# Kernel optimization log

Measured on AMD Instinct MI355X. Metric: run time of the kernel, lower is better.

Reference implementation:

```python
import jax, jax.numpy as jnp
import numpy as np

D_MODEL = 2048
N_Q_HEADS = 32
N_KV_HEADS = 8
D_HEAD = 64
D_MLP = 8192
NORM_EPS = 1e-5
INIT_RANGE = 0.02
IGNORE = -100000.0
B, S = 2, 2048


def setup_inputs() -> dict:
    key = jax.random.key(0)
    ks = jax.random.split(key, 8)
    return {
        "resid_pre": jax.random.normal(ks[0], (B, S, D_MODEL), dtype=jnp.float32),
        "W_Q": jax.random.normal(ks[1], (N_Q_HEADS, D_MODEL, D_HEAD), dtype=jnp.float32) * INIT_RANGE,
        "W_K": jax.random.normal(ks[2], (N_KV_HEADS, D_MODEL, D_HEAD), dtype=jnp.float32) * INIT_RANGE,
        "W_V": jax.random.normal(ks[3], (N_KV_HEADS, D_MODEL, D_HEAD), dtype=jnp.float32) * INIT_RANGE,
        "W_O": jax.random.normal(ks[4], (N_KV_HEADS, D_HEAD, D_MODEL), dtype=jnp.float32) * INIT_RANGE,
        "g1": jnp.ones((D_MODEL,), jnp.float32),
        "b1": jnp.zeros((D_MODEL,), jnp.float32),
        "g2": jnp.ones((D_MODEL,), jnp.float32),
        "b2": jnp.zeros((D_MODEL,), jnp.float32),
        "W_in": jax.random.normal(ks[5], (D_MODEL, D_MLP), dtype=jnp.float32) * INIT_RANGE,
        "b_in": jnp.zeros((D_MLP,), jnp.float32),
        "W_out": jax.random.normal(ks[6], (D_MLP, D_MODEL), dtype=jnp.float32) * INIT_RANGE,
        "b_out": jnp.zeros((D_MODEL,), jnp.float32),
    }


def rmsnorm(x, g, b):
    # torch.var (unbiased=False) is mean-centered variance, but x itself is
    # divided (not centered) -- faithful to the source.
    mu = jnp.mean(x, axis=-1, keepdims=True)
    var = jnp.mean(jnp.square(x - mu), axis=-1, keepdims=True)
    std = jnp.sqrt(var + NORM_EPS)
    return (x / std) * g + b


def attention(x, W_Q, W_K, W_V, W_O):
    b, s, _ = x.shape
    q = jnp.einsum('bpd,hde->bphe', x, W_Q)            # [b, s, n_q, d_head]
    k = jnp.einsum('bpd,hde->bphe', x, W_K)            # [b, s, n_kv, d_head]
    v = jnp.einsum('bpd,hde->bphe', x, W_V)            # [b, s, n_kv, d_head]
    g_size = N_Q_HEADS // N_KV_HEADS
    # rearrange '(n_kv g) d' with n_kv outer, group inner
    q = q.reshape(b, s, N_KV_HEADS, g_size, D_HEAD)
    # source einsum sums over the group dim (g not in output) -- faithful
    scores = jnp.einsum('bqkgd,bskd->bkqs', q, k) / jnp.sqrt(jnp.float32(D_HEAD))
    mask = jnp.triu(jnp.ones((s, s), dtype=bool), k=1)
    scores = jnp.where(mask, jnp.float32(IGNORE), scores)
    pattern = jax.nn.softmax(scores, axis=-1)          # [b, n_kv, q, s]
    z = jnp.einsum('bskd,bkqs->bqkd', v, pattern)      # [b, q, n_kv, d_head]
    return jnp.einsum('bqkd,kde->bqe', z, W_O)


def ffn(x, W_in, b_in, W_out, b_out):
    pre = jnp.einsum('bpd,dm->bpm', x, W_in) + b_in
    post = jax.nn.relu(pre)
    return jnp.einsum('bpm,md->bpd', post, W_out) + b_out


def reference(resid_pre, W_Q, W_K, W_V, W_O, g1, b1, g2, b2, W_in, b_in, W_out, b_out):
    resid_mid = attention(rmsnorm(resid_pre, g1, b1), W_Q, W_K, W_V, W_O) + resid_pre
    resid_post = ffn(rmsnorm(resid_mid, g2, b2), W_in, b_in, W_out, b_out) + resid_mid
    return resid_post
```

## Files before the change

### kernel.cpp

```cpp
#include <hip/hip_runtime.h>
#include <hip/hip_bf16.h>


using bf16 = __hip_bfloat16;
typedef __bf16 bf16x8_t __attribute__((ext_vector_type(8)));
typedef float  f32x4_t  __attribute__((ext_vector_type(4)));

#define D_MODEL 2048
#define SEQ     2048
#define NB      2
#define NTOK    4096
#define NKV     8
#define DHEAD   64
#define DMLP    8192
#define NQKV    1536

__device__ inline void storev(float* p, float v) { *p = v; }
__device__ inline void storev(bf16* p, float v)  { *p = __float2bfloat16(v); }

__device__ inline __bf16 tobf(float x) {
    union { __hip_bfloat16 h; __bf16 b; } u;
    u.h = __float2bfloat16(x);
    return u.b;
}

__global__ __launch_bounds__(256) void transpose_f32_bf16_kernel(
    const float* __restrict__ in, bf16* __restrict__ out, int K, int N)
{
    __shared__ float tile[32][33];
    const int n0 = blockIdx.x * 32, k0 = blockIdx.y * 32;
    const int tx = threadIdx.x & 31, ty = threadIdx.x >> 5;
    #pragma unroll
    for (int i = 0; i < 32; i += 8)
        tile[ty + i][tx] = in[(size_t)(k0 + ty + i) * N + n0 + tx];
    __syncthreads();
    #pragma unroll
    for (int i = 0; i < 32; i += 8)
        out[(size_t)(n0 + ty + i) * K + k0 + tx] = __float2bfloat16(tile[tx][ty + i]);
}

__global__ __launch_bounds__(256) void head_transpose_kernel(
    const float* __restrict__ in, bf16* __restrict__ out, int ngroup)
{
    __shared__ float tile[32][65];
    const int kv = blockIdx.y;
    const int k0 = blockIdx.x * 32;
    const int t  = threadIdx.x;
    const int e  = t & 63, kk = t >> 6;
    #pragma unroll
    for (int i = 0; i < 32; i += 4) {
        float s = 0.f;
        for (int g = 0; g < ngroup; ++g)
            s += in[((size_t)(kv * ngroup + g) * 2048 + k0 + kk + i) * 64 + e];
        tile[kk + i][e] = s;
    }
    __syncthreads();
    const int k = t & 31, ee = t >> 5;
    #pragma unroll
    for (int i = 0; i < 64; i += 8)
        out[(size_t)(kv * 64 + ee + i) * 2048 + k0 + k] = __float2bfloat16(tile[k][ee + i]);
}

__global__ __launch_bounds__(256) void rmsnorm_kernel(
    const float* __restrict__ x, const float* __restrict__ g,
    const float* __restrict__ b, bf16* __restrict__ out)
{
    const int row = blockIdx.x;
    const int t = threadIdx.x;
    const float* xr = x + (size_t)row * D_MODEL;
    float4 a0 = *reinterpret_cast<const float4*>(xr + t * 8);
    float4 a1 = *reinterpret_cast<const float4*>(xr + t * 8 + 4);
    float v[8] = {a0.x, a0.y, a0.z, a0.w, a1.x, a1.y, a1.z, a1.w};
    float sum = 0.f, sumsq = 0.f;
    #pragma unroll
    for (int j = 0; j < 8; ++j) { sum += v[j]; sumsq += v[j] * v[j]; }
    #pragma unroll
    for (int o = 1; o < 64; o <<= 1) {
        sum   += __shfl_xor(sum, o);
        sumsq += __shfl_xor(sumsq, o);
    }
    __shared__ float rs[4], rq[4];
    if ((t & 63) == 0) { rs[t >> 6] = sum; rq[t >> 6] = sumsq; }
    __syncthreads();
    sum   = rs[0] + rs[1] + rs[2] + rs[3];
    sumsq = rq[0] + rq[1] + rq[2] + rq[3];
    const float mu  = sum * (1.f / D_MODEL);
    const float var = sumsq * (1.f / D_MODEL) - mu * mu;
    const float rstd = 1.f / sqrtf(var + 1e-5f);
    const int c = t * 8;
    float4 g0 = *reinterpret_cast<const float4*>(g + c);
    float4 g1 = *reinterpret_cast<const float4*>(g + c + 4);
    float4 b0 = *reinterpret_cast<const float4*>(b + c);
    float4 b1 = *reinterpret_cast<const float4*>(b + c + 4);
    float gg[8] = {g0.x, g0.y, g0.z, g0.w, g1.x, g1.y, g1.z, g1.w};
    float bb[8] = {b0.x, b0.y, b0.z, b0.w, b1.x, b1.y, b1.z, b1.w};
    bf16* op = out + (size_t)row * D_MODEL + c;
    #pragma unroll
    for (int j = 0; j < 8; ++j) op[j] = __float2bfloat16(v[j] * rstd * gg[j] + bb[j]);
}

template<int BM, int BN, typename TC, bool BIAS, bool RELU, bool RESID>
__global__ __launch_bounds__(512, 2) void gemm_pipe_kernel(
    const bf16* __restrict__ A, const bf16* __restrict__ Bt,
    TC* __restrict__ C, const float* __restrict__ bias,
    const float* __restrict__ resid, int M, int N, int K, int nbx)
{
    constexpr int BK   = 64;
    constexpr int MREP = BM / 32;
    constexpr int NREP = BN / 64;
    constexpr int AI   = (BM * BK) / 4096;
    constexpr int BI   = (BN * BK) / 4096;
    constexpr int LD   = AI + BI;

    __shared__ __align__(16) bf16 As[2][BM * BK];
    __shared__ __align__(16) bf16 Bs[2][BN * BK];

    const int nwg = gridDim.x;
    const int swz = (blockIdx.x & 7) * (nwg >> 3) + (blockIdx.x >> 3);
    const int nby = nwg / nbx;
    const int by  = swz % nby;
    const int bx  = swz / nby;
    const int row0 = by * BM, col0 = bx * BN;

    const int t  = threadIdx.x;
    const int w  = t >> 6, ln = t & 63;
    const int wm = w >> 2, wn = w & 3;
    const int lr = ln & 15, hi = ln >> 4;

    const int srow = w * 8 + (ln >> 3);
    const int skx  = ((ln & 7) ^ (ln >> 3)) * 8;

    f32x4_t acc[MREP][NREP];
    #pragma unroll
    for (int m = 0; m < MREP; ++m)
        #pragma unroll
        for (int n = 0; n < NREP; ++n) acc[m][n] = (f32x4_t){0.f, 0.f, 0.f, 0.f};

    const int NT = K / BK;

    {
        const bf16* ga = A  + (size_t)(row0 + srow) * K + skx;
        const bf16* gb = Bt + (size_t)(col0 + srow) * K + skx;
        #pragma unroll
        for (int i = 0; i < AI; ++i)
            __builtin_amdgcn_global_load_lds(
                (const __attribute__((address_space(1))) void*)(ga + (size_t)i * 64 * K),
                (__attribute__((address_space(3))) void*)(&As[0][i * 4096 + w * 512]), 16, 0, 0);
        #pragma unroll
        for (int i = 0; i < BI; ++i)
            __builtin_amdgcn_global_load_lds(
                (const __attribute__((address_space(1))) void*)(gb + (size_t)i * 64 * K),
                (__attribute__((address_space(3))) void*)(&Bs[0][i * 4096 + w * 512]), 16, 0, 0);
    }

    for (int tt = 0; tt < NT; ++tt) {
        const int c = tt & 1;
        asm volatile("s_waitcnt lgkmcnt(0)" ::: "memory");
        __builtin_amdgcn_sched_barrier(0);
        __builtin_amdgcn_s_barrier();
        __builtin_amdgcn_sched_barrier(0);
        if (tt + 1 < NT) {
            const int d = c ^ 1;
            const int kt = (tt + 1) * BK;
            const bf16* ga = A  + (size_t)(row0 + srow) * K + kt + skx;
            const bf16* gb = Bt + (size_t)(col0 + srow) * K + kt + skx;
            #pragma unroll
            for (int i = 0; i < AI; ++i)
                __builtin_amdgcn_global_load_lds(
                    (const __attribute__((address_space(1))) void*)(ga + (size_t)i * 64 * K),
                    (__attribute__((address_space(3))) void*)(&As[d][i * 4096 + w * 512]), 16, 0, 0);
            #pragma unroll
            for (int i = 0; i < BI; ++i)
                __builtin_amdgcn_global_load_lds(
                    (const __attribute__((address_space(1))) void*)(gb + (size_t)i * 64 * K),
                    (__attribute__((address_space(3))) void*)(&Bs[d][i * 4096 + w * 512]), 16, 0, 0);
            __builtin_amdgcn_sched_barrier(0);
            if constexpr (LD == 8)      asm volatile("s_waitcnt vmcnt(8)" ::: "memory");
            else if constexpr (LD == 6) asm volatile("s_waitcnt vmcnt(6)" ::: "memory");
            else                        asm volatile("s_waitcnt vmcnt(4)" ::: "memory");
        } else {
            asm volatile("s_waitcnt vmcnt(0)" ::: "memory");
        }
        __builtin_amdgcn_sched_barrier(0);
        __builtin_amdgcn_s_barrier();
        __builtin_amdgcn_sched_barrier(0);

        #pragma unroll
        for (int kk = 0; kk < 2; ++kk) {
            bf16x8_t af[MREP], bfr[NREP];
            #pragma unroll
            for (int m = 0; m < MREP; ++m) {
                const int row = wm * (BM / 2) + m * 16 + lr;
                af[m] = *reinterpret_cast<const bf16x8_t*>(
                    &As[c][row * 64 + ((kk * 32 + hi * 8) ^ ((row & 7) << 3))]);
            }
            #pragma unroll
            for (int n = 0; n < NREP; ++n) {
                const int col = wn * (BN / 4) + n * 16 + lr;
                bfr[n] = *reinterpret_cast<const bf16x8_t*>(
                    &Bs[c][col * 64 + ((kk * 32 + hi * 8) ^ ((col & 7) << 3))]);
            }
            #pragma unroll
            for (int m = 0; m < MREP; ++m)
                #pragma unroll
                for (int n = 0; n < NREP; ++n)
                    acc[m][n] = __builtin_amdgcn_mfma_f32_16x16x32_bf16(af[m], bfr[n], acc[m][n], 0, 0, 0);
        }
    }

    #pragma unroll
    for (int m = 0; m < MREP; ++m) {
        #pragma unroll
        for (int n = 0; n < NREP; ++n) {
            const int cgl = col0 + wn * (BN / 4) + n * 16 + lr;
            #pragma unroll
            for (int j = 0; j < 4; ++j) {
                const int r = row0 + wm * (BM / 2) + m * 16 + hi * 4 + j;
                float v = acc[m][n][j];
                if constexpr (BIAS)  v += bias[cgl];
                if constexpr (RELU)  v = fmaxf(v, 0.f);
                if constexpr (RESID) v += resid[(size_t)r * N + cgl];
                storev(&C[(size_t)r * N + cgl], v);
            }
        }
    }
}

template<typename TC, bool BIAS, bool RELU, bool RESID>
__global__ __launch_bounds__(512, 2) void gemm_8ph_kernel(
    const bf16* __restrict__ A, const bf16* __restrict__ Bt,
    TC* __restrict__ C, const float* __restrict__ bias,
    const float* __restrict__ resid, int M, int N, int K, int nbx)
{
    __shared__ __align__(16) bf16 As[2][256 * 64];
    __shared__ __align__(16) bf16 Bs[2][256 * 64];

    const int nwg = gridDim.x;
    const int swz = (blockIdx.x & 7) * (nwg >> 3) + (blockIdx.x >> 3);
    const int nby = nwg / nbx;
    const int by  = swz % nby;
    const int bx  = swz / nby;
    const int row0 = by * 256, col0 = bx * 256;

    const int t  = threadIdx.x;
    const int w  = t >> 6, ln = t & 63;
    const int wm = w >> 2, wn = w & 3;
    const int lr = ln & 15, hi = ln >> 4;
    const int rx = (lr & 7) << 3;

    const int srow = w * 8 + (ln >> 3);
    const int skx  = ((ln & 7) ^ (ln >> 3)) * 8;

#define STAGE_A8(u, dbuf, kt)                                                   \
    __builtin_amdgcn_global_load_lds(                                           \
        (const __attribute__((address_space(1))) void*)(A + (size_t)(row0 + (u) * 64 + srow) * K + (kt) + skx), \
        (__attribute__((address_space(3))) void*)(&As[dbuf][(u) * 4096 + w * 512]), 16, 0, 0)
#define STAGE_B8(u, dbuf, kt)                                                   \
    __builtin_amdgcn_global_load_lds(                                           \
        (const __attribute__((address_space(1))) void*)(Bt + (size_t)(col0 + (u) * 64 + srow) * K + (kt) + skx), \
        (__attribute__((address_space(3))) void*)(&Bs[dbuf][(u) * 4096 + w * 512]), 16, 0, 0)
#define PH_BAR                                                                  \
    __builtin_amdgcn_sched_barrier(0);                                          \
    __builtin_amdgcn_s_barrier();                                               \
    __builtin_amdgcn_sched_barrier(0)
#define LGKM0                                                                   \
    asm volatile("s_waitcnt lgkmcnt(0)" ::: "memory");                          \
    __builtin_amdgcn_sched_barrier(0)

    f32x4_t acc[8][4];
    #pragma unroll
    for (int m = 0; m < 8; ++m)
        #pragma unroll
        for (int n = 0; n < 4; ++n) acc[m][n] = (f32x4_t){0.f, 0.f, 0.f, 0.f};

    bf16x8_t af[4][2];
    bf16x8_t bfr[4][2];

    const int NT = K / 64;

    STAGE_A8(0, 0, 0); STAGE_A8(2, 0, 0);
    STAGE_B8(0, 0, 0); STAGE_B8(1, 0, 0); STAGE_B8(2, 0, 0); STAGE_B8(3, 0, 0);
    STAGE_A8(1, 0, 0); STAGE_A8(3, 0, 0);
    asm volatile("s_waitcnt vmcnt(2)" ::: "memory");
    PH_BAR;

    for (int tt = 0; tt < NT; ++tt) {
        const int c  = tt & 1, d = c ^ 1;
        const int kn = (tt + 1) * 64;
        const bool pf = (tt + 1 < NT);

        #pragma unroll
        for (int mq = 0; mq < 4; ++mq) {
            const int row = wm * 128 + mq * 16 + lr;
            #pragma unroll
            for (int kk = 0; kk < 2; ++kk)
                af[mq][kk] = *reinterpret_cast<const bf16x8_t*>(
                    &As[c][row * 64 + ((kk * 32 + hi * 8) ^ rx)]);
        }
        #pragma unroll
        for (int n = 0; n < 2; ++n) {
            const int col = wn * 64 + n * 16 + lr;
            #pragma unroll
            for (int kk = 0; kk < 2; ++kk)
                bfr[n][kk] = *reinterpret_cast<const bf16x8_t*>(
                    &Bs[c][col * 64 + ((kk * 32 + hi * 8) ^ rx)]);
        }
        if (pf) { STAGE_A8(0, d, kn); STAGE_A8(2, d, kn); }
        PH_BAR;
        LGKM0;
        __builtin_amdgcn_s_setprio(1);
        #pragma unroll
        for (int mq = 0; mq < 4; ++mq)
            #pragma unroll
            for (int n = 0; n < 2; ++n)
                #pragma unroll
                for (int kk = 0; kk < 2; ++kk)
                    acc[mq][n] = __builtin_amdgcn_mfma_f32_16x16x32_bf16(af[mq][kk], bfr[n][kk], acc[mq][n], 0, 0, 0);
        __builtin_amdgcn_s_setprio(0);
        PH_BAR;

        #pragma unroll
        for (int n = 2; n < 4; ++n) {
            const int col = wn * 64 + n * 16 + lr;
            #pragma unroll
            for (int kk = 0; kk < 2; ++kk)
                bfr[n][kk] = *reinterpret_cast<const bf16x8_t*>(
                    &Bs[c][col * 64 + ((kk * 32 + hi * 8) ^ rx)]);
        }
        if (pf) { STAGE_B8(0, d, kn); STAGE_B8(1, d, kn); }
        __builtin_amdgcn_sched_barrier(0);
        if (pf) { asm volatile("s_waitcnt vmcnt(4)" ::: "memory"); }
        else    { asm volatile("s_waitcnt vmcnt(0)" ::: "memory"); }
        PH_BAR;
        LGKM0;
        __builtin_amdgcn_s_setprio(1);
        #pragma unroll
        for (int mq = 0; mq < 4; ++mq)
            #pragma unroll
            for (int n = 2; n < 4; ++n)
                #pragma unroll
                for (int kk = 0; kk < 2; ++kk)
                    acc[mq][n] = __builtin_amdgcn_mfma_f32_16x16x32_bf16(af[mq][kk], bfr[n][kk], acc[mq][n], 0, 0, 0);
        __builtin_amdgcn_s_setprio(0);
        PH_BAR;

        #pragma unroll
        for (int mq = 0; mq < 4; ++mq) {
            const int row = wm * 128 + 64 + mq * 16 + lr;
            #pragma unroll
            for (int kk = 0; kk < 2; ++kk)
                af[mq][kk] = *reinterpret_cast<const bf16x8_t*>(
                    &As[c][row * 64 + ((kk * 32 + hi * 8) ^ rx)]);
        }
        if (pf) { STAGE_B8(2, d, kn); STAGE_B8(3, d, kn); }
        PH_BAR;
        LGKM0;
        __builtin_amdgcn_s_setprio(1);
        #pragma unroll
        for (int mq = 0; mq < 4; ++mq)
            #pragma unroll
            for (int n = 2; n < 4; ++n)
                #pragma unroll
                for (int kk = 0; kk < 2; ++kk)
                    acc[4 + mq][n] = __builtin_amdgcn_mfma_f32_16x16x32_bf16(af[mq][kk], bfr[n][kk], acc[4 + mq][n], 0, 0, 0);
        __builtin_amdgcn_s_setprio(0);
        PH_BAR;

        if (pf) {
            STAGE_A8(1, d, kn); STAGE_A8(3, d, kn);
            __builtin_amdgcn_sched_barrier(0);
            asm volatile("s_waitcnt vmcnt(2)" ::: "memory");
        }
        PH_BAR;
        __builtin_amdgcn_s_setprio(1);
        #pragma unroll
        for (int mq = 0; mq < 4; ++mq)
            #pragma unroll
            for (int n = 0; n < 2; ++n)
                #pragma unroll
                for (int kk = 0; kk < 2; ++kk)
                    acc[4 + mq][n] = __builtin_amdgcn_mfma_f32_16x16x32_bf16(af[mq][kk], bfr[n][kk], acc[4 + mq][n], 0, 0, 0);
        __builtin_amdgcn_s_setprio(0);
        PH_BAR;
    }

    #pragma unroll
    for (int m = 0; m < 8; ++m) {
        #pragma unroll
        for (int n = 0; n < 4; ++n) {
            const int cgl = col0 + wn * 64 + n * 16 + lr;
            #pragma unroll
            for (int j = 0; j < 4; ++j) {
                const int r = row0 + wm * 128 + m * 16 + hi * 4 + j;
                float v = acc[m][n][j];
                if constexpr (BIAS)  v += bias[cgl];
                if constexpr (RELU)  v = fmaxf(v, 0.f);
                if constexpr (RESID) v += resid[(size_t)r * N + cgl];
                storev(&C[(size_t)r * N + cgl], v);
            }
        }
    }
#undef STAGE_A8
#undef STAGE_B8
#undef PH_BAR
#undef LGKM0
}

#define QBLK  128
#define KVBLK 64
#define LP    72

__global__ __launch_bounds__(512) void mfma_attn_kernel(
    const float* __restrict__ qkv, bf16* __restrict__ z)
{
    const int qt = blockIdx.x;
    const int kv = blockIdx.y;
    const int b  = blockIdx.z;
    const int t  = threadIdx.x;
    const int w  = t >> 6;
    const int ln = t & 63;
    const int lr = ln & 15;
    const int hi = ln >> 4;
    const int lk = hi * 8;

    __shared__ __align__(16) bf16 Ks[KVBLK * LP];
    __shared__ __align__(16) bf16 Vt[DHEAD * LP];
    __shared__ __align__(16) bf16 Ps[QBLK * LP];

    bf16x8_t qf[2];
    {
        const int qrow = qt * QBLK + w * 16 + lr;
        const float* qp = qkv + (size_t)(b * SEQ + qrow) * NQKV + kv * 64;
        #pragma unroll
        for (int kk = 0; kk < 2; ++kk) {
            float4 x0 = *reinterpret_cast<const float4*>(qp + kk * 32 + lk);
            float4 x1 = *reinterpret_cast<const float4*>(qp + kk * 32 + lk + 4);
            bf16x8_t v;
            v[0] = tobf(x0.x); v[1] = tobf(x0.y); v[2] = tobf(x0.z); v[3] = tobf(x0.w);
            v[4] = tobf(x1.x); v[5] = tobf(x1.y); v[6] = tobf(x1.z); v[7] = tobf(x1.w);
            qf[kk] = v;
        }
    }

    f32x4_t acc_o[4];
    #pragma unroll
    for (int n = 0; n < 4; ++n) acc_o[n] = (f32x4_t){0.f, 0.f, 0.f, 0.f};
    float m_st[4] = {-1e30f, -1e30f, -1e30f, -1e30f};
    float l_st[4] = {0.f, 0.f, 0.f, 0.f};

    const int qbase_cd = qt * QBLK + w * 16 + hi * 4;

    const int n_tiles = 2 * qt + 2;
    for (int kt = 0; kt < n_tiles; ++kt) {
        const int k0g = kt * KVBLK;
        __syncthreads();
        {
            const int r  = t >> 3;
            const int c8 = (t & 7) * 8;
            const float* kb = qkv + (size_t)(b * SEQ + k0g + r) * NQKV + 512 + kv * 64 + c8;
            float4 k0 = *reinterpret_cast<const float4*>(kb);
            float4 k1 = *reinterpret_cast<const float4*>(kb + 4);
            bf16x8_t kvv;
            kvv[0] = tobf(k0.x); kvv[1] = tobf(k0.y); kvv[2] = tobf(k0.z); kvv[3] = tobf(k0.w);
            kvv[4] = tobf(k1.x); kvv[5] = tobf(k1.y); kvv[6] = tobf(k1.z); kvv[7] = tobf(k1.w);
            *reinterpret_cast<bf16x8_t*>(&Ks[r * LP + c8]) = kvv;
        }
        {
            const int dv = w * 8;
            const float* vb = qkv + (size_t)(b * SEQ + k0g + ln) * NQKV + 1024 + kv * 64 + dv;
            float4 v0 = *reinterpret_cast<const float4*>(vb);
            float4 v1 = *reinterpret_cast<const float4*>(vb + 4);
            float vv[8] = {v0.x, v0.y, v0.z, v0.w, v1.x, v1.y, v1.z, v1.w};
            #pragma unroll
            for (int i = 0; i < 8; ++i)
                Vt[(dv + i) * LP + ln] = __float2bfloat16(vv[i]);
        }
        __syncthreads();

        f32x4_t s[4];
        #pragma unroll
        for (int n = 0; n < 4; ++n) s[n] = (f32x4_t){0.f, 0.f, 0.f, 0.f};
        #pragma unroll
        for (int kk = 0; kk < 2; ++kk) {
            #pragma unroll
            for (int n = 0; n < 4; ++n) {
                bf16x8_t kf = *reinterpret_cast<const bf16x8_t*>(&Ks[(n * 16 + lr) * LP + kk * 32 + lk]);
                s[n] = __builtin_amdgcn_mfma_f32_16x16x32_bf16(qf[kk], kf, s[n], 0, 0, 0);
            }
        }

        const bool need_mask = (kt >= 2 * qt);
        #pragma unroll
        for (int n = 0; n < 4; ++n) {
            const int colg = k0g + n * 16 + lr;
            #pragma unroll
            for (int j = 0; j < 4; ++j) {
                float val = s[n][j] * 0.125f;
                if (need_mask && colg > qbase_cd + j) val = -1e30f;
                s[n][j] = val;
            }
        }

        float alpha[4], mnew[4];
        #pragma unroll
        for (int j = 0; j < 4; ++j) {
            float mx = fmaxf(fmaxf(s[0][j], s[1][j]), fmaxf(s[2][j], s[3][j]));
            mx = fmaxf(mx, __shfl_xor(mx, 1));
            mx = fmaxf(mx, __shfl_xor(mx, 2));
            mx = fmaxf(mx, __shfl_xor(mx, 4));
            mx = fmaxf(mx, __shfl_xor(mx, 8));
            mnew[j]  = fmaxf(m_st[j], mx);
            alpha[j] = __expf(m_st[j] - mnew[j]);
            m_st[j]  = mnew[j];
        }
        float psum[4] = {0.f, 0.f, 0.f, 0.f};
        #pragma unroll
        for (int n = 0; n < 4; ++n) {
            #pragma unroll
            for (int j = 0; j < 4; ++j) {
                float p = __expf(s[n][j] - mnew[j]);
                psum[j] += p;
                Ps[(w * 16 + hi * 4 + j) * LP + n * 16 + lr] = __float2bfloat16(p);
            }
        }
        #pragma unroll
        for (int j = 0; j < 4; ++j) {
            float ps = psum[j];
            ps += __shfl_xor(ps, 1);
            ps += __shfl_xor(ps, 2);
            ps += __shfl_xor(ps, 4);
            ps += __shfl_xor(ps, 8);
            l_st[j] = l_st[j] * alpha[j] + ps;
        }
        #pragma unroll
        for (int n = 0; n < 4; ++n)
            #pragma unroll
            for (int j = 0; j < 4; ++j)
                acc_o[n][j] *= alpha[j];

        #pragma unroll
        for (int kk = 0; kk < 2; ++kk) {
            bf16x8_t pa = *reinterpret_cast<const bf16x8_t*>(&Ps[(w * 16 + lr) * LP + kk * 32 + lk]);
            #pragma unroll
            for (int n = 0; n < 4; ++n) {
                bf16x8_t vf = *reinterpret_cast<const bf16x8_t*>(&Vt[(n * 16 + lr) * LP + kk * 32 + lk]);
                acc_o[n] = __builtin_amdgcn_mfma_f32_16x16x32_bf16(pa, vf, acc_o[n], 0, 0, 0);
            }
        }
    }

    #pragma unroll
    for (int j = 0; j < 4; ++j) {
        const float inv = 1.f / l_st[j];
        const int tok = b * SEQ + qbase_cd + j;
        bf16* zp = z + (size_t)tok * (NKV * DHEAD) + kv * 64;
        #pragma unroll
        for (int n = 0; n < 4; ++n)
            zp[n * 16 + lr] = __float2bfloat16(acc_o[n][j] * inv);
    }
}

extern "C" void kernel_launch(void* const* d_in, const int* in_sizes, int n_in,
                              void* d_out, int out_size, void* d_ws, size_t ws_size,
                              hipStream_t stream)
{
    const float* resid_pre = (const float*)d_in[0];
    const float* W_Q   = (const float*)d_in[1];
    const float* W_K   = (const float*)d_in[2];
    const float* W_V   = (const float*)d_in[3];
    const float* W_O   = (const float*)d_in[4];
    const float* g1    = (const float*)d_in[5];
    const float* b1    = (const float*)d_in[6];
    const float* g2    = (const float*)d_in[7];
    const float* b2    = (const float*)d_in[8];
    const float* W_in  = (const float*)d_in[9];
    const float* b_in  = (const float*)d_in[10];
    const float* W_out = (const float*)d_in[11];
    const float* b_out = (const float*)d_in[12];
    float* out = (float*)d_out;

    char* ws = (char*)d_ws;
    const size_t OFF_WBIG  = 0;
    const size_t OFF_WOT   = OFF_WBIG + (size_t)DMLP * D_MODEL * 2;
    const size_t OFF_X1    = OFF_WOT  + (size_t)D_MODEL * 512 * 2;
    const size_t OFF_RMID  = OFF_X1   + (size_t)NTOK * D_MODEL * 2;
    const size_t OFF_POST  = OFF_RMID + (size_t)NTOK * D_MODEL * 4;
    const size_t OFF_WQKVT = OFF_POST;
    const size_t OFF_QKV   = OFF_WQKVT + (size_t)NQKV * D_MODEL * 2;
    const size_t OFF_Z     = OFF_QKV   + (size_t)NTOK * NQKV * 4;

    bf16*  winT   = (bf16*) (ws + OFF_WBIG);
    bf16*  woutT  = (bf16*) (ws + OFF_WBIG);
    bf16*  woT    = (bf16*) (ws + OFF_WOT);
    bf16*  x1     = (bf16*) (ws + OFF_X1);
    float* rmid   = (float*)(ws + OFF_RMID);
    bf16*  post   = (bf16*) (ws + OFF_POST);
    bf16*  wqkvT  = (bf16*) (ws + OFF_WQKVT);
    float* qkv    = (float*)(ws + OFF_QKV);
    bf16*  zbuf   = (bf16*) (ws + OFF_Z);

    transpose_f32_bf16_kernel<<<dim3(DMLP / 32, D_MODEL / 32), 256, 0, stream>>>(W_in, winT, D_MODEL, DMLP);
    head_transpose_kernel<<<dim3(D_MODEL / 32, NKV), 256, 0, stream>>>(W_Q, wqkvT, 4);
    head_transpose_kernel<<<dim3(D_MODEL / 32, NKV), 256, 0, stream>>>(W_K, wqkvT + (size_t)512  * D_MODEL, 1);
    head_transpose_kernel<<<dim3(D_MODEL / 32, NKV), 256, 0, stream>>>(W_V, wqkvT + (size_t)1024 * D_MODEL, 1);
    transpose_f32_bf16_kernel<<<dim3(D_MODEL / 32, 512 / 32), 256, 0, stream>>>(W_O, woT, 512, D_MODEL);

    rmsnorm_kernel<<<NTOK, 256, 0, stream>>>(resid_pre, g1, b1, x1);
    gemm_pipe_kernel<128, 128, float, false, false, false><<<384, 512, 0, stream>>>(
        x1, wqkvT, qkv, nullptr, nullptr, NTOK, NQKV, D_MODEL, NQKV / 128);
    mfma_attn_kernel<<<dim3(SEQ / QBLK, NKV, NB), 512, 0, stream>>>(qkv, zbuf);
    gemm_pipe_kernel<128, 128, float, false, false, true><<<512, 512, 0, stream>>>(
        zbuf, woT, rmid, nullptr, resid_pre, NTOK, D_MODEL, 512, D_MODEL / 128);
    rmsnorm_kernel<<<NTOK, 256, 0, stream>>>(rmid, g2, b2, x1);
    gemm_8ph_kernel<bf16, true, true, false><<<512, 512, 0, stream>>>(
        x1, winT, post, b_in, nullptr, NTOK, DMLP, D_MODEL, DMLP / 256);
    transpose_f32_bf16_kernel<<<dim3(D_MODEL / 32, DMLP / 32), 256, 0, stream>>>(W_out, woutT, DMLP, D_MODEL);
    gemm_pipe_kernel<128, 128, float, true, false, true><<<512, 512, 0, stream>>>(
        post, woutT, out, b_out, rmid, NTOK, D_MODEL, DMLP, D_MODEL / 128);
}
```

Before: 510.6 us.

## Pair causal query tiles in attention and use 8-phase GEMM for FFN out

```diff
diff --git a/kernel.cpp b/kernel.cpp
--- a/kernel.cpp
+++ b/kernel.cpp
@@ -226,21 +226,25 @@
     }
 }
 
-template<typename TC, bool BIAS, bool RELU, bool RESID>
+template<int BN, typename TC, bool BIAS, bool RELU, bool RESID>
 __global__ __launch_bounds__(512, 2) void gemm_8ph_kernel(
     const bf16* __restrict__ A, const bf16* __restrict__ Bt,
     TC* __restrict__ C, const float* __restrict__ bias,
     const float* __restrict__ resid, int M, int N, int K, int nbx)
 {
+    constexpr int NREP = BN / 64;
+    constexpr int NH   = NREP / 2;
+    constexpr int BI   = BN / 64;
+
     __shared__ __align__(16) bf16 As[2][256 * 64];
-    __shared__ __align__(16) bf16 Bs[2][256 * 64];
+    __shared__ __align__(16) bf16 Bs[2][BN * 64];
 
     const int nwg = gridDim.x;
     const int swz = (blockIdx.x & 7) * (nwg >> 3) + (blockIdx.x >> 3);
     const int nby = nwg / nbx;
     const int by  = swz % nby;
     const int bx  = swz / nby;
-    const int row0 = by * 256, col0 = bx * 256;
+    const int row0 = by * 256, col0 = bx * BN;
 
     const int t  = threadIdx.x;
     const int w  = t >> 6, ln = t & 63;
@@ -267,19 +271,20 @@
     asm volatile("s_waitcnt lgkmcnt(0)" ::: "memory");                          \
     __builtin_amdgcn_sched_barrier(0)
 
-    f32x4_t acc[8][4];
+    f32x4_t acc[8][NREP];
     #pragma unroll
     for (int m = 0; m < 8; ++m)
         #pragma unroll
-        for (int n = 0; n < 4; ++n) acc[m][n] = (f32x4_t){0.f, 0.f, 0.f, 0.f};
+        for (int n = 0; n < NREP; ++n) acc[m][n] = (f32x4_t){0.f, 0.f, 0.f, 0.f};
 
     bf16x8_t af[4][2];
-    bf16x8_t bfr[4][2];
+    bf16x8_t bfr[NREP][2];
 
     const int NT = K / 64;
 
     STAGE_A8(0, 0, 0); STAGE_A8(2, 0, 0);
-    STAGE_B8(0, 0, 0); STAGE_B8(1, 0, 0); STAGE_B8(2, 0, 0); STAGE_B8(3, 0, 0);
+    #pragma unroll
+    for (int u = 0; u < BI; ++u) STAGE_B8(u, 0, 0);
     STAGE_A8(1, 0, 0); STAGE_A8(3, 0, 0);
     asm volatile("s_waitcnt vmcnt(2)" ::: "memory");
     PH_BAR;
@@ -298,8 +303,8 @@
                     &As[c][row * 64 + ((kk * 32 + hi * 8) ^ rx)]);
         }
         #pragma unroll
-        for (int n = 0; n < 2; ++n) {
-            const int col = wn * 64 + n * 16 + lr;
+        for (int n = 0; n < NH; ++n) {
+            const int col = wn * (BN / 4) + n * 16 + lr;
             #pragma unroll
             for (int kk = 0; kk < 2; ++kk)
                 bfr[n][kk] = *reinterpret_cast<const bf16x8_t*>(
@@ -312,7 +317,7 @@
         #pragma unroll
         for (int mq = 0; mq < 4; ++mq)
             #pragma unroll
-            for (int n = 0; n < 2; ++n)
+            for (int n = 0; n < NH; ++n)
                 #pragma unroll
                 for (int kk = 0; kk < 2; ++kk)
                     acc[mq][n] = __builtin_amdgcn_mfma_f32_16x16x32_bf16(af[mq][kk], bfr[n][kk], acc[mq][n], 0, 0, 0);
@@ -320,8 +325,8 @@
         PH_BAR;
 
         #pragma unroll
-        for (int n = 2; n < 4; ++n) {
-            const int col = wn * 64 + n * 16 + lr;
+        for (int n = NH; n < NREP; ++n) {
+            const int col = wn * (BN / 4) + n * 16 + lr;
             #pragma unroll
             for (int kk = 0; kk < 2; ++kk)
                 bfr[n][kk] = *reinterpret_cast<const bf16x8_t*>(
@@ -337,7 +342,7 @@
         #pragma unroll
         for (int mq = 0; mq < 4; ++mq)
             #pragma unroll
-            for (int n = 2; n < 4; ++n)
+            for (int n = NH; n < NREP; ++n)
                 #pragma unroll
                 for (int kk = 0; kk < 2; ++kk)
                     acc[mq][n] = __builtin_amdgcn_mfma_f32_16x16x32_bf16(af[mq][kk], bfr[n][kk], acc[mq][n], 0, 0, 0);
@@ -352,14 +357,14 @@
                 af[mq][kk] = *reinterpret_cast<const bf16x8_t*>(
                     &As[c][row * 64 + ((kk * 32 + hi * 8) ^ rx)]);
         }
-        if (pf) { STAGE_B8(2, d, kn); STAGE_B8(3, d, kn); }
+        if (pf) { if constexpr (BI == 4) { STAGE_B8(2, d, kn); STAGE_B8(3, d, kn); } }
         PH_BAR;
         LGKM0;
         __builtin_amdgcn_s_setprio(1);
         #pragma unroll
         for (int mq = 0; mq < 4; ++mq)
             #pragma unroll
-            for (int n = 2; n < 4; ++n)
+            for (int n = NH; n < NREP; ++n)
                 #pragma unroll
                 for (int kk = 0; kk < 2; ++kk)
                     acc[4 + mq][n] = __builtin_amdgcn_mfma_f32_16x16x32_bf16(af[mq][kk], bfr[n][kk], acc[4 + mq][n], 0, 0, 0);
@@ -376,7 +381,7 @@
         #pragma unroll
         for (int mq = 0; mq < 4; ++mq)
             #pragma unroll
-            for (int n = 0; n < 2; ++n)
+            for (int n = 0; n < NH; ++n)
                 #pragma unroll
                 for (int kk = 0; kk < 2; ++kk)
                     acc[4 + mq][n] = __builtin_amdgcn_mfma_f32_16x16x32_bf16(af[mq][kk], bfr[n][kk], acc[4 + mq][n], 0, 0, 0);
@@ -387,8 +392,8 @@
     #pragma unroll
     for (int m = 0; m < 8; ++m) {
         #pragma unroll
-        for (int n = 0; n < 4; ++n) {
-            const int cgl = col0 + wn * 64 + n * 16 + lr;
+        for (int n = 0; n < NREP; ++n) {
+            const int cgl = col0 + wn * (BN / 4) + n * 16 + lr;
             #pragma unroll
             for (int j = 0; j < 4; ++j) {
                 const int r = row0 + wm * 128 + m * 16 + hi * 4 + j;
@@ -406,16 +411,16 @@
 #undef LGKM0
 }
 
-#define QBLK  128
 #define KVBLK 64
 #define LP    72
 
-__global__ __launch_bounds__(512) void mfma_attn_kernel(
+__global__ __launch_bounds__(256) void mfma_attn_kernel(
     const float* __restrict__ qkv, bf16* __restrict__ z)
 {
-    const int qt = blockIdx.x;
+    const int a  = blockIdx.x;
     const int kv = blockIdx.y;
     const int b  = blockIdx.z;
+    const int b2 = 31 - a;
     const int t  = threadIdx.x;
     const int w  = t >> 6;
     const int ln = t & 63;
@@ -425,11 +430,12 @@
 
     __shared__ __align__(16) bf16 Ks[KVBLK * LP];
     __shared__ __align__(16) bf16 Vt[DHEAD * LP];
-    __shared__ __align__(16) bf16 Ps[QBLK * LP];
-
-    bf16x8_t qf[2];
-    {
-        const int qrow = qt * QBLK + w * 16 + lr;
+    __shared__ __align__(16) bf16 Ps[64 * LP];
+
+    bf16x8_t qfA[2], qfB[2];
+    #pragma unroll
+    for (int sb = 0; sb < 2; ++sb) {
+        const int qrow = (sb ? b2 : a) * 64 + w * 16 + lr;
         const float* qp = qkv + (size_t)(b * SEQ + qrow) * NQKV + kv * 64;
         #pragma unroll
         for (int kk = 0; kk < 2; ++kk) {
@@ -438,45 +444,24 @@
             bf16x8_t v;
             v[0] = tobf(x0.x); v[1] = tobf(x0.y); v[2] = tobf(x0.z); v[3] = tobf(x0.w);
             v[4] = tobf(x1.x); v[5] = tobf(x1.y); v[6] = tobf(x1.z); v[7] = tobf(x1.w);
-            qf[kk] = v;
-        }
-    }
-
-    f32x4_t acc_o[4];
-    #pragma unroll
-    for (int n = 0; n < 4; ++n) acc_o[n] = (f32x4_t){0.f, 0.f, 0.f, 0.f};
-    float m_st[4] = {-1e30f, -1e30f, -1e30f, -1e30f};
-    float l_st[4] = {0.f, 0.f, 0.f, 0.f};
-
-    const int qbase_cd = qt * QBLK + w * 16 + hi * 4;
-
-    const int n_tiles = 2 * qt + 2;
-    for (int kt = 0; kt < n_tiles; ++kt) {
-        const int k0g = kt * KVBLK;
-        __syncthreads();
-        {
-            const int r  = t >> 3;
-            const int c8 = (t & 7) * 8;
-            const float* kb = qkv + (size_t)(b * SEQ + k0g + r) * NQKV + 512 + kv * 64 + c8;
-            float4 k0 = *reinterpret_cast<const float4*>(kb);
-            float4 k1 = *reinterpret_cast<const float4*>(kb + 4);
-            bf16x8_t kvv;
-            kvv[0] = tobf(k0.x); kvv[1] = tobf(k0.y); kvv[2] = tobf(k0.z); kvv[3] = tobf(k0.w);
-            kvv[4] = tobf(k1.x); kvv[5] = tobf(k1.y); kvv[6] = tobf(k1.z); kvv[7] = tobf(k1.w);
-            *reinterpret_cast<bf16x8_t*>(&Ks[r * LP + c8]) = kvv;
-        }
-        {
-            const int dv = w * 8;
-            const float* vb = qkv + (size_t)(b * SEQ + k0g + ln) * NQKV + 1024 + kv * 64 + dv;
-            float4 v0 = *reinterpret_cast<const float4*>(vb);
-            float4 v1 = *reinterpret_cast<const float4*>(vb + 4);
-            float vv[8] = {v0.x, v0.y, v0.z, v0.w, v1.x, v1.y, v1.z, v1.w};
-            #pragma unroll
-            for (int i = 0; i < 8; ++i)
-                Vt[(dv + i) * LP + ln] = __float2bfloat16(vv[i]);
-        }
-        __syncthreads();
-
+            if (sb) qfB[kk] = v; else qfA[kk] = v;
+        }
+    }
+
+    f32x4_t accA[4], accB[4];
+    #pragma unroll
+    for (int n = 0; n < 4; ++n) {
+        accA[n] = (f32x4_t){0.f, 0.f, 0.f, 0.f};
+        accB[n] = (f32x4_t){0.f, 0.f, 0.f, 0.f};
+    }
+    float mA[4] = {-1e30f, -1e30f, -1e30f, -1e30f}, lA[4] = {0.f, 0.f, 0.f, 0.f};
+    float mB[4] = {-1e30f, -1e30f, -1e30f, -1e30f}, lB[4] = {0.f, 0.f, 0.f, 0.f};
+
+    const int qcdA = a  * 64 + w * 16 + hi * 4;
+    const int qcdB = b2 * 64 + w * 16 + hi * 4;
+
+    auto process = [&](const bf16x8_t* qf, f32x4_t* acc_o, float* m_st,
+                       float* l_st, int qcd, int k0g, bool diag) {
         f32x4_t s[4];
         #pragma unroll
         for (int n = 0; n < 4; ++n) s[n] = (f32x4_t){0.f, 0.f, 0.f, 0.f};
@@ -488,19 +473,16 @@
                 s[n] = __builtin_amdgcn_mfma_f32_16x16x32_bf16(qf[kk], kf, s[n], 0, 0, 0);
             }
         }
-
-        const bool need_mask = (kt >= 2 * qt);
         #pragma unroll
         for (int n = 0; n < 4; ++n) {
             const int colg = k0g + n * 16 + lr;
             #pragma unroll
             for (int j = 0; j < 4; ++j) {
                 float val = s[n][j] * 0.125f;
-                if (need_mask && colg > qbase_cd + j) val = -1e30f;
+                if (diag && colg > qcd + j) val = -1e30f;
                 s[n][j] = val;
             }
         }
-
         float alpha[4], mnew[4];
         #pragma unroll
         for (int j = 0; j < 4; ++j) {
@@ -537,7 +519,6 @@
             #pragma unroll
             for (int j = 0; j < 4; ++j)
                 acc_o[n][j] *= alpha[j];
-
         #pragma unroll
         for (int kk = 0; kk < 2; ++kk) {
             bf16x8_t pa = *reinterpret_cast<const bf16x8_t*>(&Ps[(w * 16 + lr) * LP + kk * 32 + lk]);
@@ -547,16 +528,54 @@
                 acc_o[n] = __builtin_amdgcn_mfma_f32_16x16x32_bf16(pa, vf, acc_o[n], 0, 0, 0);
             }
         }
+    };
+
+    for (int kt = 0; kt <= b2; ++kt) {
+        const int k0g = kt * KVBLK;
+        __syncthreads();
+        {
+            const int r   = t >> 2;
+            const int c16 = (t & 3) * 16;
+            const float* kb = qkv + (size_t)(b * SEQ + k0g + r) * NQKV + 512 + kv * 64 + c16;
+            #pragma unroll
+            for (int h = 0; h < 2; ++h) {
+                float4 k0 = *reinterpret_cast<const float4*>(kb + h * 8);
+                float4 k1 = *reinterpret_cast<const float4*>(kb + h * 8 + 4);
+                bf16x8_t kvv;
+                kvv[0] = tobf(k0.x); kvv[1] = tobf(k0.y); kvv[2] = tobf(k0.z); kvv[3] = tobf(k0.w);
+                kvv[4] = tobf(k1.x); kvv[5] = tobf(k1.y); kvv[6] = tobf(k1.z); kvv[7] = tobf(k1.w);
+                *reinterpret_cast<bf16x8_t*>(&Ks[r * LP + c16 + h * 8]) = kvv;
+            }
+        }
+        {
+            const int dv = w * 16;
+            const float* vb = qkv + (size_t)(b * SEQ + k0g + ln) * NQKV + 1024 + kv * 64 + dv;
+            #pragma unroll
+            for (int h = 0; h < 4; ++h) {
+                float4 v4 = *reinterpret_cast<const float4*>(vb + h * 4);
+                Vt[(dv + h * 4 + 0) * LP + ln] = __float2bfloat16(v4.x);
+                Vt[(dv + h * 4 + 1) * LP + ln] = __float2bfloat16(v4.y);
+                Vt[(dv + h * 4 + 2) * LP + ln] = __float2bfloat16(v4.z);
+                Vt[(dv + h * 4 + 3) * LP + ln] = __float2bfloat16(v4.w);
+            }
+        }
+        __syncthreads();
+
+        if (kt <= a) process(qfA, accA, mA, lA, qcdA, k0g, kt == a);
+        process(qfB, accB, mB, lB, qcdB, k0g, kt == b2);
     }
 
     #pragma unroll
     for (int j = 0; j < 4; ++j) {
-        const float inv = 1.f / l_st[j];
-        const int tok = b * SEQ + qbase_cd + j;
-        bf16* zp = z + (size_t)tok * (NKV * DHEAD) + kv * 64;
-        #pragma unroll
-        for (int n = 0; n < 4; ++n)
-            zp[n * 16 + lr] = __float2bfloat16(acc_o[n][j] * inv);
+        const float invA = 1.f / lA[j];
+        bf16* zpA = z + (size_t)(b * SEQ + qcdA + j) * (NKV * DHEAD) + kv * 64;
+        const float invB = 1.f / lB[j];
+        bf16* zpB = z + (size_t)(b * SEQ + qcdB + j) * (NKV * DHEAD) + kv * 64;
+        #pragma unroll
+        for (int n = 0; n < 4; ++n) {
+            zpA[n * 16 + lr] = __float2bfloat16(accA[n][j] * invA);
+            zpB[n * 16 + lr] = __float2bfloat16(accB[n][j] * invB);
+        }
     }
 }
 
@@ -608,13 +627,13 @@
     rmsnorm_kernel<<<NTOK, 256, 0, stream>>>(resid_pre, g1, b1, x1);
     gemm_pipe_kernel<128, 128, float, false, false, false><<<384, 512, 0, stream>>>(
         x1, wqkvT, qkv, nullptr, nullptr, NTOK, NQKV, D_MODEL, NQKV / 128);
-    mfma_attn_kernel<<<dim3(SEQ / QBLK, NKV, NB), 512, 0, stream>>>(qkv, zbuf);
+    mfma_attn_kernel<<<dim3(16, NKV, NB), 256, 0, stream>>>(qkv, zbuf);
     gemm_pipe_kernel<128, 128, float, false, false, true><<<512, 512, 0, stream>>>(
         zbuf, woT, rmid, nullptr, resid_pre, NTOK, D_MODEL, 512, D_MODEL / 128);
     rmsnorm_kernel<<<NTOK, 256, 0, stream>>>(rmid, g2, b2, x1);
-    gemm_8ph_kernel<bf16, true, true, false><<<512, 512, 0, stream>>>(
+    gemm_8ph_kernel<256, bf16, true, true, false><<<512, 512, 0, stream>>>(
         x1, winT, post, b_in, nullptr, NTOK, DMLP, D_MODEL, DMLP / 256);
     transpose_f32_bf16_kernel<<<dim3(D_MODEL / 32, DMLP / 32), 256, 0, stream>>>(W_out, woutT, DMLP, D_MODEL);
-    gemm_pipe_kernel<128, 128, float, true, false, true><<<512, 512, 0, stream>>>(
+    gemm_8ph_kernel<128, float, true, false, true><<<256, 512, 0, stream>>>(
         post, woutT, out, b_out, rmid, NTOK, D_MODEL, DMLP, D_MODEL / 128);
 }
```

New measurement: 535.5 us. 4.9% more time.
